# Kernel tuning notes

Hardware: AMD Instinct MI355X
Metric: run time of the kernel (lower is better)

Reference implementation:

```python
import jax, jax.numpy as jnp
import numpy as np

HIDDEN = 4096
N_HEADS = 32
N_KV_HEADS = 8
HEAD_DIM = HIDDEN // N_HEADS  # 128
ROPE_THETA = 10000.0
BATCH, SEQ = 2, 2048


def setup_inputs() -> dict:
    key = jax.random.key(0)
    ks = jax.random.split(key, 5)
    s = 0.02
    return {
        "hidden_states": jax.random.normal(ks[0], (BATCH, SEQ, HIDDEN), jnp.float32),
        "position_ids": jnp.broadcast_to(jnp.arange(SEQ, dtype=jnp.int32), (BATCH, SEQ)),
        "Wq": jax.random.normal(ks[1], (HIDDEN, HIDDEN), jnp.float32) * s,
        "Wk": jax.random.normal(ks[2], (N_KV_HEADS * HEAD_DIM, HIDDEN), jnp.float32) * s,
        "Wv": jax.random.normal(ks[3], (N_KV_HEADS * HEAD_DIM, HIDDEN), jnp.float32) * s,
        "Wo": jax.random.normal(ks[4], (HIDDEN, HIDDEN), jnp.float32) * s,
    }


def _rope_cos_sin(position_ids, dtype):
    # HF LlamaRotaryEmbedding: inv_freq over even dims, emb = concat(freqs, freqs)
    inv_freq = 1.0 / (ROPE_THETA ** (jnp.arange(0, HEAD_DIM, 2, dtype=jnp.float32) / HEAD_DIM))
    freqs = position_ids.astype(jnp.float32)[..., None] * inv_freq[None, None, :]  # [B,S,D/2]
    emb = jnp.concatenate([freqs, freqs], axis=-1)  # [B,S,D]
    return jnp.cos(emb).astype(dtype), jnp.sin(emb).astype(dtype)


def _rotate_half(x):
    x1, x2 = jnp.split(x, 2, axis=-1)
    return jnp.concatenate([-x2, x1], axis=-1)


def reference(hidden_states, position_ids, Wq, Wk, Wv, Wo):
    B, S, _ = hidden_states.shape
    dtype = hidden_states.dtype

    # QKV projections (nn.Linear: x @ W.T), reshape to [B, H, S, D]
    q = (hidden_states @ Wq.T).reshape(B, S, N_HEADS, HEAD_DIM).transpose(0, 2, 1, 3)
    k = (hidden_states @ Wk.T).reshape(B, S, N_KV_HEADS, HEAD_DIM).transpose(0, 2, 1, 3)
    v = (hidden_states @ Wv.T).reshape(B, S, N_KV_HEADS, HEAD_DIM).transpose(0, 2, 1, 3)

    # RoPE
    cos, sin = _rope_cos_sin(position_ids, dtype)  # [B,S,D]
    cos_b, sin_b = cos[:, None, :, :], sin[:, None, :, :]
    q = q * cos_b + _rotate_half(q) * sin_b
    k = k * cos_b + _rotate_half(k) * sin_b

    # GQA: group queries over shared kv heads instead of materializing repeat_kv
    groups = N_HEADS // N_KV_HEADS
    qg = q.reshape(B, N_KV_HEADS, groups, S, HEAD_DIM)

    scale = 1.0 / jnp.sqrt(jnp.asarray(HEAD_DIM, dtype=jnp.float32)).astype(dtype)
    scores = jnp.einsum('bkgqd,bkld->bkgql', qg, k) * scale  # [B,KV,G,S,S]

    causal = jnp.tril(jnp.ones((S, S), dtype=bool))
    scores = jnp.where(causal[None, None, None], scores, jnp.asarray(-jnp.inf, scores.dtype))
    probs = jax.nn.softmax(scores.astype(jnp.float32), axis=-1).astype(dtype)

    out = jnp.einsum('bkgql,bkld->bkgqd', probs, v)  # [B,KV,G,S,D]
    out = out.reshape(B, N_HEADS, S, HEAD_DIM).transpose(0, 2, 1, 3).reshape(B, S, HIDDEN)
    return out @ Wo.T
```

## Files before the change

### kernel.cpp

```cpp
#include <hip/hip_runtime.h>
#include <cstdint>
#include <cstddef>

typedef unsigned short u16;
typedef short bf16x8 __attribute__((ext_vector_type(8)));
typedef float f32x4 __attribute__((ext_vector_type(4)));

#define HIDDEN 4096
#define NH 32
#define NKV 8
#define HD 128
#define SEQL 2048
#define BATCH 2
#define NTOK (BATCH*SEQL)
#define QKVN (HIDDEN + 2*NKV*HD)

#define QKS 68

__device__ __forceinline__ u16 f2bf(float f){
    unsigned u = __float_as_uint(f);
    u += 0x7FFF + ((u >> 16) & 1);
    return (u16)(u >> 16);
}
__device__ __forceinline__ float bf2f(u16 h){
    return __uint_as_float(((unsigned)h) << 16);
}
__device__ __forceinline__ f32x4 zero4(){
    f32x4 z; z[0]=0.f; z[1]=0.f; z[2]=0.f; z[3]=0.f; return z;
}

typedef const unsigned int __attribute__((address_space(1)))* gas1_t;
typedef unsigned int __attribute__((address_space(3)))* las3_t;
__device__ __forceinline__ void gload_lds16(const u16* g, u16* l){
    __builtin_amdgcn_global_load_lds((gas1_t)g, (las3_t)l, 16, 0, 0);
}

__global__ __launch_bounds__(256) void cvt_kernel(const float* __restrict__ src,
                                                  u16* __restrict__ dst, int n4){
    int i = blockIdx.x * 256 + threadIdx.x;
    if (i < n4){
        float4 v = ((const float4*)src)[i];
        ushort4 o;
        o.x = f2bf(v.x); o.y = f2bf(v.y); o.z = f2bf(v.z); o.w = f2bf(v.w);
        ((ushort4*)dst)[i] = o;
    }
}

template<int OUT_BF16>
__global__ __launch_bounds__(256) void gemm4_bt(const u16* __restrict__ A,
                                                const u16* __restrict__ B,
                                                void* __restrict__ Cp,
                                                int M, int N, int K){
    __shared__ __align__(16) u16 L[2][2][128*64];
    int tid = threadIdx.x;
    int wave = tid >> 6, lane = tid & 63, quad = lane >> 4, l16 = lane & 15;
    int wm = wave >> 1, wn = wave & 1;

    int nwg = gridDim.x;
    int cpx = nwg >> 3;
    int orig = blockIdx.x;
    int wg = (orig & 7) * cpx + (orig >> 3);
    int nbx = N >> 7;
    int bx = wg % nbx, by = wg / nbx;
    size_t row0 = (size_t)by * 128, col0 = (size_t)bx * 128;

    int r0 = tid >> 3, cc = (tid & 7) ^ (r0 & 7);
    const u16* aS0 = A + (row0 + r0) * (size_t)K + cc * 8;
    const u16* bS0 = B + (col0 + r0) * (size_t)K + cc * 8;
    u16* ldsd = &L[0][0][0] + tid * 8;

#define STAGE_MAT(mat, bufi, kt) do {                                               \
        const u16* g_ = ((mat) ? bS0 : aS0) + (size_t)(kt) * 64;                    \
        u16* d_ = ldsd + (bufi)*16384 + (mat)*8192;                                 \
        gload_lds16(g_,                       d_);                                  \
        gload_lds16(g_ + (size_t)32 * K,      d_ + 2048);                           \
        gload_lds16(g_ + (size_t)64 * K,      d_ + 4096);                           \
        gload_lds16(g_ + (size_t)96 * K,      d_ + 6144);                           \
    } while(0)

    const int nt = K >> 6;

    int swz0 = ((0*4 + quad) ^ (l16 & 7)) * 8;
    int swz1 = ((1*4 + quad) ^ (l16 & 7)) * 8;

    f32x4 acc[4][4];
    #pragma unroll
    for (int i=0;i<4;i++)
        #pragma unroll
        for (int j=0;j<4;j++) acc[i][j] = zero4();

    STAGE_MAT(1, 0, 0);
    STAGE_MAT(0, 0, 0);
    STAGE_MAT(1, 1, 1);

    bf16x8 bF[4][2];
    for (int t = 0; t < nt; ++t){
        if (t < nt - 1) asm volatile("s_waitcnt vmcnt(4)" ::: "memory");
        else            asm volatile("s_waitcnt vmcnt(0)" ::: "memory");
        __builtin_amdgcn_s_barrier();
        const u16* bufA = &L[t & 1][0][0];
        const u16* bufB = &L[t & 1][1][0];

        #pragma unroll
        for (int p = 0; p < 2; ++p){
            bf16x8 aF[2][2];
            if (p == 0){
                #pragma unroll
                for (int ni = 0; ni < 4; ++ni){
                    int rb = (wn*64 + ni*16 + l16) * 64;
                    bF[ni][0] = *(const bf16x8*)(bufB + rb + swz0);
                    bF[ni][1] = *(const bf16x8*)(bufB + rb + swz1);
                }
            }
            #pragma unroll
            for (int i = 0; i < 2; ++i){
                int ra = (wm*64 + p*32 + i*16 + l16) * 64;
                aF[i][0] = *(const bf16x8*)(bufA + ra + swz0);
                aF[i][1] = *(const bf16x8*)(bufA + ra + swz1);
            }
            if (p == 0){ if (t + 1 < nt) STAGE_MAT(0, (t+1)&1, t+1); }
            if (p == 1){ if (t + 2 < nt) STAGE_MAT(1, t&1, t+2); }

            __builtin_amdgcn_sched_barrier(0);
            __builtin_amdgcn_s_barrier();
            __builtin_amdgcn_sched_barrier(0);
            __builtin_amdgcn_s_setprio(1);
            #pragma unroll
            for (int ni = 0; ni < 4; ++ni)
                #pragma unroll
                for (int i = 0; i < 2; ++i){
                    acc[p*2+i][ni] = __builtin_amdgcn_mfma_f32_16x16x32_bf16(aF[i][0], bF[ni][0], acc[p*2+i][ni], 0, 0, 0);
                    acc[p*2+i][ni] = __builtin_amdgcn_mfma_f32_16x16x32_bf16(aF[i][1], bF[ni][1], acc[p*2+i][ni], 0, 0, 0);
                }
            __builtin_amdgcn_s_setprio(0);
            __builtin_amdgcn_sched_barrier(0);
            asm volatile("s_waitcnt lgkmcnt(0)" ::: "memory");
            if (p == 0) __builtin_amdgcn_s_barrier();
        }
    }
#undef STAGE_MAT

    #pragma unroll
    for (int mi = 0; mi < 4; ++mi)
        #pragma unroll
        for (int ni = 0; ni < 4; ++ni){
            size_t row = row0 + wm*64 + mi*16 + quad*4;
            size_t col = col0 + wn*64 + ni*16 + l16;
            #pragma unroll
            for (int r = 0; r < 4; ++r){
                if (OUT_BF16) ((u16*)Cp)[(row + r) * (size_t)N + col] = f2bf(acc[mi][ni][r]);
                else          ((float*)Cp)[(row + r) * (size_t)N + col] = acc[mi][ni][r];
            }
        }
}

template<int OUT_BF16>
__global__ __launch_bounds__(512) void gemm8_bt(const u16* __restrict__ A,
                                                const u16* __restrict__ B,
                                                void* __restrict__ Cp,
                                                int M, int N, int K){
    __shared__ __align__(16) u16 L[2][2][256*64];
    int tid = threadIdx.x;
    int wave = tid >> 6, lane = tid & 63, quad = lane >> 4, l16 = lane & 15;
    int wm = wave >> 2, wn = wave & 3;

    int nwg = gridDim.x;
    int cpx = nwg >> 3;
    int orig = blockIdx.x;
    int wg = (orig & 7) * cpx + (orig >> 3);
    int nbx = N >> 8;
    int bx = wg % nbx, by = wg / nbx;
    size_t row0 = (size_t)by * 256, col0 = (size_t)bx * 256;

    int r0 = tid >> 3, cc = (tid & 7) ^ (r0 & 7);
    const u16* aS0 = A + (row0 + r0) * (size_t)K + cc * 8;
    const u16* bS0 = B + (col0 + r0) * (size_t)K + cc * 8;
    u16* ldsd = &L[0][0][0] + tid * 8;

#define STAGE_HALF(mat, half, bufi, kt) do {                                        \
        const u16* g_ = ((mat) ? bS0 : aS0) + (size_t)((half)*128) * K + (size_t)(kt) * 64; \
        u16* d_ = ldsd + (bufi)*32768 + (mat)*16384 + (half)*8192;                  \
        gload_lds16(g_, d_);                                                        \
        gload_lds16(g_ + (size_t)64 * K, d_ + 4096);                                \
    } while(0)

    const int nt = K >> 6;

    int swz0 = ((0*4 + quad) ^ (l16 & 7)) * 8;
    int swz1 = ((1*4 + quad) ^ (l16 & 7)) * 8;

    f32x4 acc[8][4];
    #pragma unroll
    for (int i=0;i<8;i++)
        #pragma unroll
        for (int j=0;j<4;j++) acc[i][j] = zero4();

    STAGE_HALF(1,0,0,0); STAGE_HALF(1,1,0,0);
    STAGE_HALF(0,0,0,0); STAGE_HALF(0,1,0,0);
    STAGE_HALF(1,0,1,1); STAGE_HALF(1,1,1,1);

    bf16x8 bF[4][2];
    for (int t = 0; t < nt; ++t){
        if (t < nt - 1) asm volatile("s_waitcnt vmcnt(4)" ::: "memory");
        else            asm volatile("s_waitcnt vmcnt(0)" ::: "memory");
        __builtin_amdgcn_s_barrier();
        const u16* bufA = &L[t & 1][0][0];
        const u16* bufB = &L[t & 1][1][0];

        #pragma unroll
        for (int p = 0; p < 4; ++p){
            bf16x8 aF[2][2];
            if (p == 0){
                #pragma unroll
                for (int ni = 0; ni < 4; ++ni){
                    int rb = (wn*64 + ni*16 + l16) * 64;
                    bF[ni][0] = *(const bf16x8*)(bufB + rb + swz0);
                    bF[ni][1] = *(const bf16x8*)(bufB + rb + swz1);
                }
            }
            #pragma unroll
            for (int i = 0; i < 2; ++i){
                int ra = (wm*128 + p*32 + i*16 + l16) * 64;
                aF[i][0] = *(const bf16x8*)(bufA + ra + swz0);
                aF[i][1] = *(const bf16x8*)(bufA + ra + swz1);
            }
            if (p == 0){ if (t + 1 < nt) STAGE_HALF(0, 0, (t+1)&1, t+1); }
            if (p == 1){ if (t + 1 < nt) STAGE_HALF(0, 1, (t+1)&1, t+1); }
            if (p == 2){ if (t + 2 < nt) STAGE_HALF(1, 0, t&1, t+2); }
            if (p == 3){ if (t + 2 < nt) STAGE_HALF(1, 1, t&1, t+2); }

            __builtin_amdgcn_sched_barrier(0);
            __builtin_amdgcn_s_barrier();
            __builtin_amdgcn_sched_barrier(0);
            __builtin_amdgcn_s_setprio(1);
            #pragma unroll
            for (int ni = 0; ni < 4; ++ni)
                #pragma unroll
                for (int i = 0; i < 2; ++i){
                    acc[p*2+i][ni] = __builtin_amdgcn_mfma_f32_16x16x32_bf16(aF[i][0], bF[ni][0], acc[p*2+i][ni], 0, 0, 0);
                    acc[p*2+i][ni] = __builtin_amdgcn_mfma_f32_16x16x32_bf16(aF[i][1], bF[ni][1], acc[p*2+i][ni], 0, 0, 0);
                }
            __builtin_amdgcn_s_setprio(0);
            __builtin_amdgcn_sched_barrier(0);
            asm volatile("s_waitcnt lgkmcnt(0)" ::: "memory");
            if (p < 3) __builtin_amdgcn_s_barrier();
        }
    }
#undef STAGE_HALF

    #pragma unroll
    for (int mi = 0; mi < 8; ++mi)
        #pragma unroll
        for (int ni = 0; ni < 4; ++ni){
            size_t row = row0 + wm*128 + mi*16 + quad*4;
            size_t col = col0 + wn*64 + ni*16 + l16;
            #pragma unroll
            for (int r = 0; r < 4; ++r){
                if (OUT_BF16) ((u16*)Cp)[(row + r) * (size_t)N + col] = f2bf(acc[mi][ni][r]);
                else          ((float*)Cp)[(row + r) * (size_t)N + col] = acc[mi][ni][r];
            }
        }
}

__global__ __launch_bounds__(256) void rope_kernel(u16* __restrict__ qkv,
                                                   const int* __restrict__ pos_ids){
    int idx = blockIdx.x * 256 + threadIdx.x;
    if (idx < 8388608){
        int tok = idx >> 11;
        int rem = idx & 2047;
        int h = rem >> 6, d = rem & 63;
        size_t base = (size_t)tok * QKVN + h * 128 + d;
        float v1 = bf2f(qkv[base]), v2 = bf2f(qkv[base + 64]);
        float p = (float)pos_ids[tok];
        float invf = exp2f((float)d * -0.2076205059304601f);
        float fr = p * invf;
        float s, c; __sincosf(fr, &s, &c);
        qkv[base]      = f2bf(v1 * c - v2 * s);
        qkv[base + 64] = f2bf(v2 * c + v1 * s);
    } else {
        int i2 = idx - 8388608;
        int tok = i2 >> 9;
        int rem = i2 & 511;
        int kv = rem >> 6, d = rem & 63;
        size_t base = (size_t)tok * QKVN + HIDDEN + kv * 128 + d;
        float v1 = bf2f(qkv[base]), v2 = bf2f(qkv[base + 64]);
        float p = (float)pos_ids[tok];
        float invf = exp2f((float)d * -0.2076205059304601f);
        float fr = p * invf;
        float s, c; __sincosf(fr, &s, &c);
        qkv[base]      = f2bf(v1 * c - v2 * s);
        qkv[base + 64] = f2bf(v2 * c + v1 * s);
    }
}

__global__ __launch_bounds__(256) void vtrans_kernel(const u16* __restrict__ qkv,
                                                     u16* __restrict__ Vt){
    int blk = blockIdx.x;
    int tt = blk & 31, bkv = blk >> 5;
    int b = bkv >> 3, kv = bkv & 7;
    const u16* src = qkv + (size_t)(b * SEQL + tt * 64) * QKVN + 5120 + kv * HD;
    u16* dst = Vt + ((size_t)(b * NKV + kv)) * HD * SEQL + tt * 64;
    int tid = threadIdx.x;
    for (int i = tid; i < 1024; i += 256){
        int d = i >> 3, sc = i & 7;
        u16 tmp[8];
        #pragma unroll
        for (int j = 0; j < 8; j++) tmp[j] = src[(size_t)(sc * 8 + j) * QKVN + d];
        *(uint4*)(dst + (size_t)d * SEQL + sc * 8) = *(const uint4*)tmp;
    }
}

__global__ __launch_bounds__(256) void attn_kernel(const u16* __restrict__ qkv,
                                                   const u16* __restrict__ Vt,
                                                   u16* __restrict__ outb){
    __shared__ __align__(16) u16 Ks[2][64*128];
    __shared__ __align__(16) u16 Vs[2][128*64];
    __shared__ __align__(16) u16 Ps[4][16*QKS];

    int qt = 31 - (blockIdx.x >> 6);
    int bh = blockIdx.x & 63;
    int h  = bh & 31;
    int b  = bh >> 5;
    int kvh = h >> 2;
    int tid = threadIdx.x, wave = tid >> 6, lane = tid & 63;
    int quad = lane >> 4, l16 = lane & 15;
    int q0 = qt * 64, qrow = q0 + wave * 16;

    const u16* Qg  = qkv + (size_t)(b * SEQL + qrow + l16) * QKVN + h * HD;
    const u16* Kg0 = qkv + (size_t)(b * SEQL) * QKVN + HIDDEN + kvh * HD;
    const u16* Vg  = Vt + ((size_t)(b * NKV + kvh)) * HD * SEQL;
    u16* Pw = &Ps[wave][0];

    const u16* kg[4]; u16* kd[4];
    const u16* vg[4]; u16* vd[4];
    {
        int r4 = lane >> 4, s16 = lane & 15;
        int r8 = lane >> 3, s8 = lane & 7;
        #pragma unroll
        for (int i = 0; i < 4; i++){
            int lr = wave * 16 + i * 4 + r4;
            int cK = s16 ^ (lr & 15);
            kg[i] = Kg0 + (size_t)lr * QKVN + cK * 8;
            kd[i] = &Ks[0][0] + lr * 128 + s16 * 8;
            int dr = wave * 32 + i * 8 + r8;
            int cV = s8 ^ (dr & 7);
            vg[i] = Vg + (size_t)dr * SEQL + cV * 8;
            vd[i] = &Vs[0][0] + dr * 64 + s8 * 8;
        }
    }

    #pragma unroll
    for (int i = 0; i < 4; i++) gload_lds16(kg[i], kd[i]);
    #pragma unroll
    for (int i = 0; i < 4; i++) gload_lds16(vg[i], vd[i]);

    const float scale = 0.08838834764831845f;
    bf16x8 qf[4];
    #pragma unroll
    for (int c = 0; c < 4; c++){
        bf16x8 q = *(const bf16x8*)(Qg + c * 32 + quad * 8);
        #pragma unroll
        for (int e = 0; e < 8; e++){
            float f = bf2f((u16)q[e]) * scale;
            q[e] = (short)f2bf(f);
        }
        qf[c] = q;
    }

    float m_i[4] = {-INFINITY, -INFINITY, -INFINITY, -INFINITY};
    float l_i[4] = {0.f, 0.f, 0.f, 0.f};
    f32x4 Oacc[8];
    #pragma unroll
    for (int t=0;t<8;t++) Oacc[t] = zero4();

    const int nt = qt + 1;
    for (int t = 0; t < nt; ++t){
        int cur = t & 1;
        __syncthreads();
        if (t + 1 < nt){
            int nxt = (t + 1) & 1;
            size_t kOff = (size_t)(t + 1) * 64 * QKVN;
            int vOff = (t + 1) * 64;
            #pragma unroll
            for (int i = 0; i < 4; i++) gload_lds16(kg[i] + kOff, kd[i] + nxt * 8192);
            #pragma unroll
            for (int i = 0; i < 4; i++) gload_lds16(vg[i] + vOff, vd[i] + nxt * 8192);
        }
        const u16* Kc = &Ks[cur][0];
        const u16* Vc = &Vs[cur][0];
        int k0 = t * 64;

        f32x4 st[4];
        #pragma unroll
        for (int s=0;s<4;s++) st[s] = zero4();
        __builtin_amdgcn_s_setprio(1);
        #pragma unroll
        for (int c4 = 0; c4 < 4; c4++){
            int cw = c4 * 4 + quad;
            #pragma unroll
            for (int s = 0; s < 4; s++){
                bf16x8 bk = *(const bf16x8*)(Kc + (s*16 + l16)*128 + (cw ^ l16)*8);
                st[s] = __builtin_amdgcn_mfma_f32_16x16x32_bf16(qf[c4], bk, st[s], 0, 0, 0);
            }
        }
        __builtin_amdgcn_s_setprio(0);

        bool needmask = (k0 + 63 >= qrow);
        int row_g = qrow + quad * 4;
        float alpha[4];
        #pragma unroll
        for (int r=0;r<4;r++){
            float mx = m_i[r];
            #pragma unroll
            for (int s=0;s<4;s++){
                float v = st[s][r];
                if (needmask){
                    int col = k0 + s*16 + l16;
                    v = (col <= row_g + r) ? v : -INFINITY;
                }
                st[s][r] = v;
                mx = fmaxf(mx, v);
            }
            #pragma unroll
            for (int m=8;m>=1;m>>=1) mx = fmaxf(mx, __shfl_xor(mx, m));
            float mnew = mx;
            alpha[r] = __expf(m_i[r] - mnew);
            float rs = 0.f;
            #pragma unroll
            for (int s=0;s<4;s++){
                float pv = __expf(st[s][r] - mnew);
                st[s][r] = pv;
                rs += pv;
            }
            #pragma unroll
            for (int m=8;m>=1;m>>=1) rs += __shfl_xor(rs, m);
            l_i[r] = l_i[r] * alpha[r] + rs;
            m_i[r] = mnew;
        }

        #pragma unroll
        for (int s=0;s<8;s++)
            #pragma unroll
            for (int r=0;r<4;r++) Oacc[s][r] *= alpha[r];

        #pragma unroll
        for (int s=0;s<4;s++)
            #pragma unroll
            for (int r=0;r<4;r++)
                Pw[(quad*4 + r)*QKS + s*16 + l16] = f2bf(st[s][r]);

        __builtin_amdgcn_s_setprio(1);
        #pragma unroll
        for (int c2 = 0; c2 < 2; c2++){
            bf16x8 ap = *(const bf16x8*)(Pw + l16*QKS + c2*32 + quad*8);
            int cw = c2 * 4 + quad;
            #pragma unroll
            for (int s = 0; s < 8; s++){
                int d = s*16 + l16;
                bf16x8 bv = *(const bf16x8*)(Vc + d*64 + (cw ^ (l16 & 7))*8);
                Oacc[s] = __builtin_amdgcn_mfma_f32_16x16x32_bf16(ap, bv, Oacc[s], 0, 0, 0);
            }
        }
        __builtin_amdgcn_s_setprio(0);
    }

    float invl[4];
    #pragma unroll
    for (int r=0;r<4;r++) invl[r] = 1.f / l_i[r];
    int row0 = qrow + quad * 4;
    #pragma unroll
    for (int s=0;s<8;s++)
        #pragma unroll
        for (int r=0;r<4;r++){
            size_t o = ((size_t)(b * SEQL + row0 + r)) * HIDDEN + h * HD + s*16 + l16;
            outb[o] = f2bf(Oacc[s][r] * invl[r]);
        }
}

extern "C" void kernel_launch(void* const* d_in, const int* in_sizes, int n_in,
                              void* d_out, int out_size, void* d_ws, size_t ws_size,
                              hipStream_t stream){
    (void)in_sizes; (void)n_in; (void)out_size; (void)ws_size;
    const float* hs  = (const float*)d_in[0];
    const int*   pos = (const int*)d_in[1];
    const float* Wq  = (const float*)d_in[2];
    const float* Wk  = (const float*)d_in[3];
    const float* Wv  = (const float*)d_in[4];
    const float* Wo  = (const float*)d_in[5];
    float* out = (float*)d_out;
    char* ws = (char*)d_ws;

    u16* Xbf  = (u16*)(ws);
    u16* Wqkv = (u16*)(ws + 33554432);
    u16* Wob  = (u16*)(ws + 83886080);
    u16* QKVb = (u16*)(ws + 117440512);
    u16* Vt   = (u16*)(ws + 167772160);
    u16* attn_bf = Xbf;

    cvt_kernel<<<16384, 256, 0, stream>>>(hs, Xbf, 4194304);
    cvt_kernel<<<16384, 256, 0, stream>>>(Wq, Wqkv, 4194304);
    cvt_kernel<<<4096,  256, 0, stream>>>(Wk, Wqkv + (size_t)4096*4096, 1048576);
    cvt_kernel<<<4096,  256, 0, stream>>>(Wv, Wqkv + (size_t)5120*4096, 1048576);
    cvt_kernel<<<16384, 256, 0, stream>>>(Wo, Wob, 4194304);

    gemm4_bt<1><<<1536, 256, 0, stream>>>(Xbf, Wqkv, QKVb, NTOK, QKVN, HIDDEN);
    rope_kernel<<<40960, 256, 0, stream>>>(QKVb, pos);
    vtrans_kernel<<<512, 256, 0, stream>>>(QKVb, Vt);
    attn_kernel<<<BATCH*NH*(SEQL/64), 256, 0, stream>>>(QKVb, Vt, attn_bf);
    gemm8_bt<0><<<256, 512, 0, stream>>>(attn_bf, Wob, out, NTOK, HIDDEN, HIDDEN);
}
```

Baseline: 815.5 us.

## Use 256x192 tiles with 512 threads for the QKV projection GEMM

```diff
diff --git a/kernel.cpp b/kernel.cpp
--- a/kernel.cpp
+++ b/kernel.cpp
@@ -46,12 +46,11 @@
     }
 }
 
-template<int OUT_BF16>
-__global__ __launch_bounds__(256) void gemm4_bt(const u16* __restrict__ A,
-                                                const u16* __restrict__ B,
-                                                void* __restrict__ Cp,
-                                                int M, int N, int K){
-    __shared__ __align__(16) u16 L[2][2][128*64];
+__global__ __launch_bounds__(512) void gemm192_bt(const u16* __restrict__ A,
+                                                  const u16* __restrict__ B,
+                                                  u16* __restrict__ Cp,
+                                                  int M, int N, int K){
+    __shared__ __align__(16) u16 L[2*28672];
     int tid = threadIdx.x;
     int wave = tid >> 6, lane = tid & 63, quad = lane >> 4, l16 = lane & 15;
     int wm = wave >> 1, wn = wave & 1;
@@ -60,22 +59,31 @@
     int cpx = nwg >> 3;
     int orig = blockIdx.x;
     int wg = (orig & 7) * cpx + (orig >> 3);
-    int nbx = N >> 7;
+    int nbx = N / 192;
     int bx = wg % nbx, by = wg / nbx;
-    size_t row0 = (size_t)by * 128, col0 = (size_t)bx * 128;
+    size_t row0 = (size_t)by * 256, col0 = (size_t)bx * 192;
 
     int r0 = tid >> 3, cc = (tid & 7) ^ (r0 & 7);
     const u16* aS0 = A + (row0 + r0) * (size_t)K + cc * 8;
     const u16* bS0 = B + (col0 + r0) * (size_t)K + cc * 8;
-    u16* ldsd = &L[0][0][0] + tid * 8;
-
-#define STAGE_MAT(mat, bufi, kt) do {                                               \
-        const u16* g_ = ((mat) ? bS0 : aS0) + (size_t)(kt) * 64;                    \
-        u16* d_ = ldsd + (bufi)*16384 + (mat)*8192;                                 \
-        gload_lds16(g_,                       d_);                                  \
-        gload_lds16(g_ + (size_t)32 * K,      d_ + 2048);                           \
-        gload_lds16(g_ + (size_t)64 * K,      d_ + 4096);                           \
-        gload_lds16(g_ + (size_t)96 * K,      d_ + 6144);                           \
+    u16* ldsd = &L[0] + tid * 8;
+
+#define STAGE_A2(bufi, kt, sw0) do {                                                \
+        const u16* g_ = aS0 + (size_t)(kt) * 64 + (size_t)((sw0)*64) * K;           \
+        u16* d_ = ldsd + (bufi)*28672 + (sw0)*4096;                                 \
+        gload_lds16(g_, d_);                                                        \
+        gload_lds16(g_ + (size_t)64 * K, d_ + 4096);                                \
+    } while(0)
+#define STAGE_B2(bufi, kt) do {                                                     \
+        const u16* g_ = bS0 + (size_t)(kt) * 64;                                    \
+        u16* d_ = ldsd + (bufi)*28672 + 16384;                                      \
+        gload_lds16(g_, d_);                                                        \
+        gload_lds16(g_ + (size_t)64 * K, d_ + 4096);                                \
+    } while(0)
+#define STAGE_B1(bufi, kt) do {                                                     \
+        const u16* g_ = bS0 + (size_t)(kt) * 64 + (size_t)128 * K;                  \
+        u16* d_ = ldsd + (bufi)*28672 + 16384 + 8192;                               \
+        gload_lds16(g_, d_);                                                        \
     } while(0)
 
     const int nt = K >> 6;
@@ -83,74 +91,73 @@
     int swz0 = ((0*4 + quad) ^ (l16 & 7)) * 8;
     int swz1 = ((1*4 + quad) ^ (l16 & 7)) * 8;
 
-    f32x4 acc[4][4];
+    f32x4 acc[4][6];
     #pragma unroll
     for (int i=0;i<4;i++)
         #pragma unroll
-        for (int j=0;j<4;j++) acc[i][j] = zero4();
-
-    STAGE_MAT(1, 0, 0);
-    STAGE_MAT(0, 0, 0);
-    STAGE_MAT(1, 1, 1);
-
-    bf16x8 bF[4][2];
+        for (int j=0;j<6;j++) acc[i][j] = zero4();
+
+    STAGE_B2(0,0); STAGE_B1(0,0);
+    STAGE_A2(0,0,0); STAGE_A2(0,0,2);
+    STAGE_B2(1,1); STAGE_B1(1,1);
+
+    bf16x8 bF[6][2];
     for (int t = 0; t < nt; ++t){
-        if (t < nt - 1) asm volatile("s_waitcnt vmcnt(4)" ::: "memory");
+        if (t < nt - 1) asm volatile("s_waitcnt vmcnt(3)" ::: "memory");
         else            asm volatile("s_waitcnt vmcnt(0)" ::: "memory");
         __builtin_amdgcn_s_barrier();
-        const u16* bufA = &L[t & 1][0][0];
-        const u16* bufB = &L[t & 1][1][0];
-
-        #pragma unroll
-        for (int p = 0; p < 2; ++p){
-            bf16x8 aF[2][2];
+        const u16* bufA = &L[(t & 1) * 28672];
+        const u16* bufB = bufA + 16384;
+
+        #pragma unroll
+        for (int p = 0; p < 4; ++p){
+            bf16x8 aF[2];
             if (p == 0){
                 #pragma unroll
-                for (int ni = 0; ni < 4; ++ni){
-                    int rb = (wn*64 + ni*16 + l16) * 64;
+                for (int ni = 0; ni < 6; ++ni){
+                    int rb = (wn*96 + ni*16 + l16) * 64;
                     bF[ni][0] = *(const bf16x8*)(bufB + rb + swz0);
                     bF[ni][1] = *(const bf16x8*)(bufB + rb + swz1);
                 }
             }
-            #pragma unroll
-            for (int i = 0; i < 2; ++i){
-                int ra = (wm*64 + p*32 + i*16 + l16) * 64;
-                aF[i][0] = *(const bf16x8*)(bufA + ra + swz0);
-                aF[i][1] = *(const bf16x8*)(bufA + ra + swz1);
-            }
-            if (p == 0){ if (t + 1 < nt) STAGE_MAT(0, (t+1)&1, t+1); }
-            if (p == 1){ if (t + 2 < nt) STAGE_MAT(1, t&1, t+2); }
+            {
+                int ra = (wm*64 + p*16 + l16) * 64;
+                aF[0] = *(const bf16x8*)(bufA + ra + swz0);
+                aF[1] = *(const bf16x8*)(bufA + ra + swz1);
+            }
+            if (p == 0){ if (t + 1 < nt) STAGE_A2((t+1)&1, t+1, 0); }
+            if (p == 1){ if (t + 1 < nt) STAGE_A2((t+1)&1, t+1, 2); }
+            if (p == 2){ if (t + 2 < nt) STAGE_B2(t&1, t+2); }
+            if (p == 3){ if (t + 2 < nt) STAGE_B1(t&1, t+2); }
 
             __builtin_amdgcn_sched_barrier(0);
             __builtin_amdgcn_s_barrier();
             __builtin_amdgcn_sched_barrier(0);
             __builtin_amdgcn_s_setprio(1);
             #pragma unroll
-            for (int ni = 0; ni < 4; ++ni)
-                #pragma unroll
-                for (int i = 0; i < 2; ++i){
-                    acc[p*2+i][ni] = __builtin_amdgcn_mfma_f32_16x16x32_bf16(aF[i][0], bF[ni][0], acc[p*2+i][ni], 0, 0, 0);
-                    acc[p*2+i][ni] = __builtin_amdgcn_mfma_f32_16x16x32_bf16(aF[i][1], bF[ni][1], acc[p*2+i][ni], 0, 0, 0);
-                }
+            for (int ni = 0; ni < 6; ++ni){
+                acc[p][ni] = __builtin_amdgcn_mfma_f32_16x16x32_bf16(aF[0], bF[ni][0], acc[p][ni], 0, 0, 0);
+                acc[p][ni] = __builtin_amdgcn_mfma_f32_16x16x32_bf16(aF[1], bF[ni][1], acc[p][ni], 0, 0, 0);
+            }
             __builtin_amdgcn_s_setprio(0);
             __builtin_amdgcn_sched_barrier(0);
             asm volatile("s_waitcnt lgkmcnt(0)" ::: "memory");
-            if (p == 0) __builtin_amdgcn_s_barrier();
-        }
-    }
-#undef STAGE_MAT
+            if (p < 3) __builtin_amdgcn_s_barrier();
+        }
+    }
+#undef STAGE_A2
+#undef STAGE_B2
+#undef STAGE_B1
 
     #pragma unroll
     for (int mi = 0; mi < 4; ++mi)
         #pragma unroll
-        for (int ni = 0; ni < 4; ++ni){
+        for (int ni = 0; ni < 6; ++ni){
             size_t row = row0 + wm*64 + mi*16 + quad*4;
-            size_t col = col0 + wn*64 + ni*16 + l16;
-            #pragma unroll
-            for (int r = 0; r < 4; ++r){
-                if (OUT_BF16) ((u16*)Cp)[(row + r) * (size_t)N + col] = f2bf(acc[mi][ni][r]);
-                else          ((float*)Cp)[(row + r) * (size_t)N + col] = acc[mi][ni][r];
-            }
+            size_t col = col0 + wn*96 + ni*16 + l16;
+            #pragma unroll
+            for (int r = 0; r < 4; ++r)
+                Cp[(row + r) * (size_t)N + col] = f2bf(acc[mi][ni][r]);
         }
 }
 
@@ -503,7 +510,7 @@
     cvt_kernel<<<4096,  256, 0, stream>>>(Wv, Wqkv + (size_t)5120*4096, 1048576);
     cvt_kernel<<<16384, 256, 0, stream>>>(Wo, Wob, 4194304);
 
-    gemm4_bt<1><<<1536, 256, 0, stream>>>(Xbf, Wqkv, QKVb, NTOK, QKVN, HIDDEN);
+    gemm192_bt<<<512, 512, 0, stream>>>(Xbf, Wqkv, QKVb, NTOK, QKVN, HIDDEN);
     rope_kernel<<<40960, 256, 0, stream>>>(QKVb, pos);
     vtrans_kernel<<<512, 256, 0, stream>>>(QKVb, Vt);
     attn_kernel<<<BATCH*NH*(SEQL/64), 256, 0, stream>>>(QKVb, Vt, attn_bf);
```

After: 769.9 us. 5.6% less time.
